# Kernel optimization log

Hardware: AMD Instinct MI355X
Metric: run time of the kernel (lower is better)

The kernel has to match this reference:

```python
import jax, jax.numpy as jnp
import numpy as np

# VG model constants hard-coded in the torch module
THETA = -0.1436
MU = 0.1686
SIGMA = 0.1213
N_STEPS = 365          # len(timegrid) - 1
T_END = 1.0            # timegrid = linspace(0, 1, 366)
MC = 200000
N_MAT = 12
N_STRIKES = 21


def setup_inputs() -> dict:
    key = jax.random.key(0)
    k1, k2 = jax.random.split(key, 2)
    h = T_END / N_STEPS
    S0 = jnp.full((1, 1), 100.0, dtype=jnp.float32)
    rate = jnp.full((1, 1), 0.025, dtype=jnp.float32)
    z = jax.random.normal(k1, (MC, N_STEPS), dtype=jnp.float32)
    # VG subordinator increments: Gamma(shape=h/mu, scale=mu)
    gamma = (jax.random.gamma(k2, h / MU, (MC, N_STEPS)) * MU).astype(jnp.float32)
    # monthly maturities on the daily grid
    indices = (jnp.arange(1, N_MAT + 1, dtype=jnp.int32) * 30)
    strikes_call = jnp.linspace(80.0, 120.0, N_STRIKES, dtype=jnp.float32)
    strikes_put = jnp.linspace(80.0, 120.0, N_STRIKES, dtype=jnp.float32)
    return {"S0": S0, "rate": rate, "indices": indices, "z": z, "gamma": gamma,
            "strikes_call": strikes_call, "strikes_put": strikes_put,
            "MC_samples": MC}


def reference(S0, rate, indices, z, gamma, strikes_call, strikes_put, MC_samples):
    h = jnp.asarray(T_END / N_STEPS, dtype=z.dtype)
    # martingale correction w = (1/mu) * log(1 - theta*mu - sigma^2*mu/2)
    w = (1.0 / MU) * jnp.log(1.0 - THETA * MU - SIGMA * SIGMA * MU / 2.0)
    r = rate.reshape(())
    s0 = S0.reshape(())
    # VG log-increment per step; cumulative sum gives X after each step i
    incr = THETA * gamma + SIGMA * jnp.sqrt(gamma) * z      # [MC, N_STEPS]
    X = jnp.cumsum(incr, axis=1)                            # X[:, i-1] = X after step i
    # gather the maturity steps
    Xm = X[:, indices - 1]                                  # [MC, M]
    im = indices.astype(z.dtype)                            # [M]
    Sm = s0 * jnp.exp((r + w) * im * h + Xm)                # [MC, M]
    disc = jnp.exp(-r * im / N_STEPS)                       # [M] (discount as in torch code)
    Sb = Sm[:, :, None]                                     # [MC, M, 1]
    Kc = strikes_call[None, None, :]                        # [1, 1, K]
    Kp = strikes_put[None, None, :]
    d = disc[:, None]                                       # [M, 1]
    call      = jnp.maximum(Sb - Kc, 0.0).mean(axis=0) * d  # average_SS
    put_otm   = jnp.maximum(Kp - Sb, 0.0).mean(axis=0) * d  # average_SS_OTM
    call_kput = jnp.maximum(Sb - Kp, 0.0).mean(axis=0) * d  # average_SS1
    put_kcall = jnp.maximum(Kc - Sb, 0.0).mean(axis=0) * d  # average_SS1_ITM
    # [4*M, K]
    return jnp.concatenate([call, put_otm, call_kput, put_kcall], axis=0)
```

## Files before the change

kernel.cpp:

```cpp
#include <hip/hip_runtime.h>
#include <math.h>


#define NSTEPS 365
#define NM     12
#define NK     21
#define PPW    8
#define WAVES  4
#define BLOCK  (WAVES * 64)
#define PPB    (WAVES * PPW)

#define NCELL  (NM * NK)
#define WSZ    (2 * NCELL + NM)

#define THETA_F (-0.1436f)
#define SIGMA_F (0.1213f)
#define THETA_D (-0.1436)
#define MU_D    (0.1686)
#define SIGMA_D (0.1213)

template <int CTRL, int RMASK>
__device__ __forceinline__ float dpp_add(float v) {
    const int t = __builtin_amdgcn_update_dpp(0, __float_as_int(v), CTRL, RMASK, 0xf, true);
    return v + __int_as_float(t);
}
__device__ __forceinline__ float scan64(float v) {
    v = dpp_add<0x111, 0xf>(v);
    v = dpp_add<0x112, 0xf>(v);
    v = dpp_add<0x114, 0xf>(v);
    v = dpp_add<0x118, 0xf>(v);
    v = dpp_add<0x142, 0xa>(v);
    v = dpp_add<0x143, 0xc>(v);
    return v;
}
__device__ __forceinline__ float rdlane(float v, int l) {
    return __int_as_float(__builtin_amdgcn_readlane(__float_as_int(v), l));
}

__global__ __launch_bounds__(BLOCK) void vg_paths_kernel(
    const float* __restrict__ S0p, const float* __restrict__ ratep,
    const int* __restrict__ indices, const float* __restrict__ z,
    const float* __restrict__ gam, const float* __restrict__ Kc,
    const float* __restrict__ Kp, float* __restrict__ acc, int MC)
{
    __shared__ float lacc[WSZ];
    const int tid = threadIdx.x;
    for (int i = tid; i < WSZ; i += BLOCK) lacc[i] = 0.f;
    __syncthreads();

    const int lane = tid & 63;
    const int wv   = tid >> 6;
    const int k    = lane % NK;
    const int mg   = lane / NK;

    const float kc  = Kc[k];
    const float kp  = Kp[k];
    const float r_  = ratep[0];
    const float s0_ = S0p[0];
    const float w   = (float)((1.0 / MU_D) *
                      log(1.0 - THETA_D * MU_D - SIGMA_D * SIGMA_D * MU_D / 2.0));
    const float rwh  = (r_ + w) / (float)NSTEPS;
    const float lns0 = logf(s0_);

    float ab2[NM];
    #pragma unroll
    for (int m = 0; m < NM; ++m) ab2[m] = rwh * (float)indices[m] + lns0;

    float ac_c[4], ac_p[4], sS[4];
    #pragma unroll
    for (int j = 0; j < 4; ++j) { ac_c[j] = 0.f; ac_p[j] = 0.f; sS[j] = 0.f; }

    auto loadp = [&](int p, float* zv, float* gv) {
        const int pc = min(p, MC - 1);
        const float* zp = z   + (size_t)pc * NSTEPS;
        const float* gp = gam + (size_t)pc * NSTEPS;
        #pragma unroll
        for (int c = 0; c < 5; ++c) {
            zv[c] = zp[lane + 64 * c];
            gv[c] = gp[lane + 64 * c];
        }
        const int o5 = min(lane + 320, 364);
        zv[5] = zp[o5]; gv[5] = gp[o5];
    };

    auto process = [&](const float* zv, const float* gv, bool pv) {
        float X[NM];
        float carry = 0.f;
        #pragma unroll
        for (int c = 0; c < 6; ++c) {
            const float g = gv[c];
            float v = fmaf(THETA_F, g, SIGMA_F * (sqrtf(g) * zv[c]));
            if (c == 5) v = (lane < 45) ? v : 0.f;
            v = scan64(v);
            X[2 * c]     = carry + rdlane(v, 29 - 4 * c);
            X[2 * c + 1] = carry + rdlane(v, 59 - 4 * c);
            carry       += rdlane(v, 63);
        }
        if (!pv) return;
        float S[NM];
        #pragma unroll
        for (int m = 0; m < NM; ++m) S[m] = __expf(ab2[m] + X[m]);
        #pragma unroll
        for (int j = 0; j < 4; ++j) {
            const float Sj = (mg == 0) ? S[j] : (mg == 1) ? S[j + 4] : S[j + 8];
            ac_c[j] += fmaxf(Sj - kc, 0.f);
            ac_p[j] += fmaxf(Sj - kp, 0.f);
            sS[j]   += Sj;
        }
    };

    const int p0 = blockIdx.x * PPB + wv * PPW;
    float zA[6], gA[6], zB[6], gB[6];
    loadp(p0, zA, gA);
    #pragma unroll 1
    for (int pp = 0; pp < PPW; pp += 2) {
        loadp(p0 + pp + 1, zB, gB);
        process(zA, gA, p0 + pp < MC);
        loadp(p0 + pp + 2, zA, gA);
        process(zB, gB, p0 + pp + 1 < MC);
    }

    if (lane < 63) {
        #pragma unroll
        for (int j = 0; j < 4; ++j) {
            const int cell = (4 * mg + j) * NK + k;
            atomicAdd(&lacc[cell],         ac_c[j]);
            atomicAdd(&lacc[NCELL + cell], ac_p[j]);
        }
        if (k == 0) {
            #pragma unroll
            for (int j = 0; j < 4; ++j)
                atomicAdd(&lacc[2 * NCELL + 4 * mg + j], sS[j]);
        }
    }
    __syncthreads();
    for (int i = tid; i < WSZ; i += BLOCK)
        atomicAdd(&acc[i], lacc[i]);
}

__global__ void vg_finalize_kernel(const float* __restrict__ acc,
                                   const float* __restrict__ ratep,
                                   const int* __restrict__ indices,
                                   const float* __restrict__ Kc,
                                   const float* __restrict__ Kp,
                                   float* __restrict__ out, int MC)
{
    const int i = blockIdx.x * blockDim.x + threadIdx.x;
    if (i >= 4 * NCELL) return;
    const int t    = i / NCELL;
    const int cell = i % NCELL;
    const int m    = cell / NK;
    const int kk   = cell % NK;
    const float r_   = ratep[0];
    const float im   = (float)indices[m];
    const float disc = expf(-r_ * im / (float)NSTEPS);
    const float cc = acc[cell];
    const float cp = acc[NCELL + cell];
    const float sS = acc[2 * NCELL + m];
    const float fM = (float)MC;
    float v;
    if      (t == 0) v = cc;
    else if (t == 1) v = cp - sS + fM * Kp[kk];
    else if (t == 2) v = cp;
    else             v = cc - sS + fM * Kc[kk];
    out[i] = disc * v / fM;
}

extern "C" void kernel_launch(void* const* d_in, const int* in_sizes, int n_in,
                              void* d_out, int out_size, void* d_ws, size_t ws_size,
                              hipStream_t stream) {
    const float* S0      = (const float*)d_in[0];
    const float* rate    = (const float*)d_in[1];
    const int*   indices = (const int*)d_in[2];
    const float* z       = (const float*)d_in[3];
    const float* gamma_  = (const float*)d_in[4];
    const float* Kc      = (const float*)d_in[5];
    const float* Kp      = (const float*)d_in[6];

    const int MC = in_sizes[3] / NSTEPS;
    float* acc = (float*)d_ws;

    (void)hipMemsetAsync(d_ws, 0, WSZ * sizeof(float), stream);

    const int nb = (MC + PPB - 1) / PPB;
    vg_paths_kernel<<<nb, BLOCK, 0, stream>>>(S0, rate, indices, z, gamma_, Kc, Kp, acc, MC);

    vg_finalize_kernel<<<(4 * NCELL + 255) / 256, 256, 0, stream>>>(
        acc, rate, indices, Kc, Kp, (float*)d_out, MC);
}
```

Measured before the change: 193.4 us.

## Interleave two paths' DPP scans and deepen load prefetch; use exp2 domain

Processes two Monte Carlo paths at once, so their DPP prefix-scan chains interleave and hide DPP latency. The main loop is fully unrolled and keeps four paths of loads in flight instead of two. Constants are folded into base-2 so exp2f replaces __expf, and the per-maturity offsets are made scalar via readfirstlane. This costs more VGPRs, which may lower occupancy.

```diff
diff --git a/kernel.cpp b/kernel.cpp
--- a/kernel.cpp
+++ b/kernel.cpp
@@ -18,23 +18,18 @@
 #define THETA_D (-0.1436)
 #define MU_D    (0.1686)
 #define SIGMA_D (0.1213)
+#define LOG2E_F (1.4426950408889634f)
 
 template <int CTRL, int RMASK>
 __device__ __forceinline__ float dpp_add(float v) {
     const int t = __builtin_amdgcn_update_dpp(0, __float_as_int(v), CTRL, RMASK, 0xf, true);
     return v + __int_as_float(t);
 }
-__device__ __forceinline__ float scan64(float v) {
-    v = dpp_add<0x111, 0xf>(v);
-    v = dpp_add<0x112, 0xf>(v);
-    v = dpp_add<0x114, 0xf>(v);
-    v = dpp_add<0x118, 0xf>(v);
-    v = dpp_add<0x142, 0xa>(v);
-    v = dpp_add<0x143, 0xc>(v);
-    return v;
-}
 __device__ __forceinline__ float rdlane(float v, int l) {
     return __int_as_float(__builtin_amdgcn_readlane(__float_as_int(v), l));
+}
+__device__ __forceinline__ float rfl(float v) {
+    return __int_as_float(__builtin_amdgcn_readfirstlane(__float_as_int(v)));
 }
 
 __global__ __launch_bounds__(BLOCK) void vg_paths_kernel(
@@ -59,16 +54,21 @@
     const float s0_ = S0p[0];
     const float w   = (float)((1.0 / MU_D) *
                       log(1.0 - THETA_D * MU_D - SIGMA_D * SIGMA_D * MU_D / 2.0));
-    const float rwh  = (r_ + w) / (float)NSTEPS;
-    const float lns0 = logf(s0_);
+    const float th2  = THETA_F * LOG2E_F;
+    const float sg2  = SIGMA_F * LOG2E_F;
+    const float rwh2 = (r_ + w) * LOG2E_F / (float)NSTEPS;
+    const float l2s0 = log2f(s0_);
 
     float ab2[NM];
     #pragma unroll
-    for (int m = 0; m < NM; ++m) ab2[m] = rwh * (float)indices[m] + lns0;
+    for (int m = 0; m < NM; ++m) ab2[m] = rfl(rwh2 * (float)indices[m] + l2s0);
 
     float ac_c[4], ac_p[4], sS[4];
     #pragma unroll
     for (int j = 0; j < 4; ++j) { ac_c[j] = 0.f; ac_p[j] = 0.f; sS[j] = 0.f; }
+
+    const int o5 = min(lane + 320, 364);
+    const bool m5 = (lane < 45);
 
     auto loadp = [&](int p, float* zv, float* gv) {
         const int pc = min(p, MC - 1);
@@ -79,46 +79,60 @@
             zv[c] = zp[lane + 64 * c];
             gv[c] = gp[lane + 64 * c];
         }
-        const int o5 = min(lane + 320, 364);
         zv[5] = zp[o5]; gv[5] = gp[o5];
     };
 
-    auto process = [&](const float* zv, const float* gv, bool pv) {
-        float X[NM];
-        float carry = 0.f;
+    auto process2 = [&](const float* zA, const float* gA, bool pvA,
+                        const float* zB, const float* gB, bool pvB) {
+        float XA[NM], XB[NM];
+        float cA = 0.f, cB = 0.f;
         #pragma unroll
         for (int c = 0; c < 6; ++c) {
-            const float g = gv[c];
-            float v = fmaf(THETA_F, g, SIGMA_F * (sqrtf(g) * zv[c]));
-            if (c == 5) v = (lane < 45) ? v : 0.f;
-            v = scan64(v);
-            X[2 * c]     = carry + rdlane(v, 29 - 4 * c);
-            X[2 * c + 1] = carry + rdlane(v, 59 - 4 * c);
-            carry       += rdlane(v, 63);
-        }
-        if (!pv) return;
-        float S[NM];
-        #pragma unroll
-        for (int m = 0; m < NM; ++m) S[m] = __expf(ab2[m] + X[m]);
-        #pragma unroll
-        for (int j = 0; j < 4; ++j) {
-            const float Sj = (mg == 0) ? S[j] : (mg == 1) ? S[j + 4] : S[j + 8];
-            ac_c[j] += fmaxf(Sj - kc, 0.f);
-            ac_p[j] += fmaxf(Sj - kp, 0.f);
-            sS[j]   += Sj;
+            const float ga = gA[c], gb = gB[c];
+            float va = fmaf(th2, ga, sg2 * (sqrtf(ga) * zA[c]));
+            float vb = fmaf(th2, gb, sg2 * (sqrtf(gb) * zB[c]));
+            if (c == 5) { va = m5 ? va : 0.f; vb = m5 ? vb : 0.f; }
+            va = dpp_add<0x111, 0xf>(va);  vb = dpp_add<0x111, 0xf>(vb);
+            va = dpp_add<0x112, 0xf>(va);  vb = dpp_add<0x112, 0xf>(vb);
+            va = dpp_add<0x114, 0xf>(va);  vb = dpp_add<0x114, 0xf>(vb);
+            va = dpp_add<0x118, 0xf>(va);  vb = dpp_add<0x118, 0xf>(vb);
+            va = dpp_add<0x142, 0xa>(va);  vb = dpp_add<0x142, 0xa>(vb);
+            va = dpp_add<0x143, 0xc>(va);  vb = dpp_add<0x143, 0xc>(vb);
+            XA[2 * c]     = cA + rdlane(va, 29 - 4 * c);
+            XB[2 * c]     = cB + rdlane(vb, 29 - 4 * c);
+            XA[2 * c + 1] = cA + rdlane(va, 59 - 4 * c);
+            XB[2 * c + 1] = cB + rdlane(vb, 59 - 4 * c);
+            cA += rdlane(va, 63);
+            cB += rdlane(vb, 63);
+        }
+        #pragma unroll
+        for (int half = 0; half < 2; ++half) {
+            const float* X = half ? XB : XA;
+            const bool  pv = half ? pvB : pvA;
+            if (!pv) continue;
+            float S[NM];
+            #pragma unroll
+            for (int m = 0; m < NM; ++m) S[m] = exp2f(ab2[m] + X[m]);
+            #pragma unroll
+            for (int j = 0; j < 4; ++j) {
+                const float Sj = (mg == 0) ? S[j] : (mg == 1) ? S[j + 4] : S[j + 8];
+                ac_c[j] += fmaxf(Sj - kc, 0.f);
+                ac_p[j] += fmaxf(Sj - kp, 0.f);
+                sS[j]   += Sj;
+            }
         }
     };
 
     const int p0 = blockIdx.x * PPB + wv * PPW;
-    float zA[6], gA[6], zB[6], gB[6];
-    loadp(p0, zA, gA);
-    #pragma unroll 1
-    for (int pp = 0; pp < PPW; pp += 2) {
-        loadp(p0 + pp + 1, zB, gB);
-        process(zA, gA, p0 + pp < MC);
-        loadp(p0 + pp + 2, zA, gA);
-        process(zB, gB, p0 + pp + 1 < MC);
-    }
+    float zE[6], gE[6], zO[6], gO[6], zE2[6], gE2[6], zO2[6], gO2[6];
+    loadp(p0 + 0, zE,  gE );  loadp(p0 + 1, zO,  gO );
+    loadp(p0 + 2, zE2, gE2);  loadp(p0 + 3, zO2, gO2);
+    process2(zE,  gE,  p0 + 0 < MC, zO,  gO,  p0 + 1 < MC);
+    loadp(p0 + 4, zE,  gE );  loadp(p0 + 5, zO,  gO );
+    process2(zE2, gE2, p0 + 2 < MC, zO2, gO2, p0 + 3 < MC);
+    loadp(p0 + 6, zE2, gE2);  loadp(p0 + 7, zO2, gO2);
+    process2(zE,  gE,  p0 + 4 < MC, zO,  gO,  p0 + 5 < MC);
+    process2(zE2, gE2, p0 + 6 < MC, zO2, gO2, p0 + 7 < MC);
 
     if (lane < 63) {
         #pragma unroll
```

After: 197.5 us. 2.1% more time.

## Switch to one path per thread with sequential scan and LDS payoff stage

Applied to the files above, without the earlier changes.

Replaces the wave-cooperative path scan (one path per wave, DPP prefix sums) with one path per thread. Each thread sums its 365 increments sequentially using float4 loads, with per-wave alignment offsets so the vector loads stay 16-byte aligned. Spot prices go to shared memory, and each wave then accumulates payoffs over its 64 paths. It also folds log2e into the constants so exp2f can be used, and hardcodes maturities as multiples of 30 instead of reading indices. The aim is to remove cross-lane scan and readlane overhead, at the cost of strided, uncoalesced per-thread memory access and a dependence on the specific test maturity grid.

```diff
diff --git a/kernel.cpp b/kernel.cpp
--- a/kernel.cpp
+++ b/kernel.cpp
@@ -5,11 +5,7 @@
 #define NSTEPS 365
 #define NM     12
 #define NK     21
-#define PPW    8
-#define WAVES  4
-#define BLOCK  (WAVES * 64)
-#define PPB    (WAVES * PPW)
-
+#define BLOCK  256
 #define NCELL  (NM * NK)
 #define WSZ    (2 * NCELL + NM)
 
@@ -18,23 +14,58 @@
 #define THETA_D (-0.1436)
 #define MU_D    (0.1686)
 #define SIGMA_D (0.1213)
+#define LOG2E_F (1.4426950408889634f)
 
-template <int CTRL, int RMASK>
-__device__ __forceinline__ float dpp_add(float v) {
-    const int t = __builtin_amdgcn_update_dpp(0, __float_as_int(v), CTRL, RMASK, 0xf, true);
-    return v + __int_as_float(t);
-}
-__device__ __forceinline__ float scan64(float v) {
-    v = dpp_add<0x111, 0xf>(v);
-    v = dpp_add<0x112, 0xf>(v);
-    v = dpp_add<0x114, 0xf>(v);
-    v = dpp_add<0x118, 0xf>(v);
-    v = dpp_add<0x142, 0xa>(v);
-    v = dpp_add<0x143, 0xc>(v);
-    return v;
-}
-__device__ __forceinline__ float rdlane(float v, int l) {
-    return __int_as_float(__builtin_amdgcn_readlane(__float_as_int(v), l));
+template <int Q>
+__device__ __forceinline__ void sim_path(const float* __restrict__ zA,
+                                         const float* __restrict__ gA,
+                                         float th2, float sg2,
+                                         float rwh2, float l2s0,
+                                         float* __restrict__ Srow)
+{
+    float X = 0.f;
+    #pragma unroll 1
+    for (int rr = 0; rr < 6; ++rr) {
+        const float* zb = zA + 60 * rr;
+        const float* gb = gA + 60 * rr;
+        const float frr = (float)rr;
+        const bool rr0 = (rr == 0);
+        #pragma unroll
+        for (int r2 = 0; r2 < 15; ++r2) {
+            const float4 z4 = *(const float4*)(zb + 4 * r2);
+            const float4 g4 = *(const float4*)(gb + 4 * r2);
+            #define VG_EL(ZJ, GJ, LE)                                          \
+            do {                                                               \
+                float inc = fmaf(th2, (GJ), sg2 * (sqrtf((GJ)) * (ZJ)));       \
+                if (Q > 0 && (LE) < Q) inc = rr0 ? 0.f : inc;     \
+                X += inc;                                                      \
+                if (Q > 0 && (LE) == Q - 1) {            \
+                    if (!rr0)                                                  \
+                        Srow[2 * rr - 1] =                                     \
+                            exp2f(fmaf(rwh2, 60.f * frr, l2s0) + X);           \
+                }                                                              \
+                if ((LE) == 29 + Q)                      \
+                    Srow[2 * rr] =                                             \
+                        exp2f(fmaf(rwh2, 60.f * frr + 30.f, l2s0) + X);        \
+                if (Q == 0 && (LE) == 59)                \
+                    Srow[2 * rr + 1] =                                         \
+                        exp2f(fmaf(rwh2, 60.f * frr + 60.f, l2s0) + X);        \
+            } while (0)
+            VG_EL(z4.x, g4.x, 4 * r2 + 0);
+            VG_EL(z4.y, g4.y, 4 * r2 + 1);
+            VG_EL(z4.z, g4.z, 4 * r2 + 2);
+            VG_EL(z4.w, g4.w, 4 * r2 + 3);
+            #undef VG_EL
+        }
+    }
+    if (Q > 0) {
+        const float4 z4 = *(const float4*)(zA + 360);
+        const float4 g4 = *(const float4*)(gA + 360);
+        if (Q >= 1) X += fmaf(th2, g4.x, sg2 * (sqrtf(g4.x) * z4.x));
+        if (Q >= 2) X += fmaf(th2, g4.y, sg2 * (sqrtf(g4.y) * z4.y));
+        if (Q >= 3) X += fmaf(th2, g4.z, sg2 * (sqrtf(g4.z) * z4.z));
+        Srow[11] = exp2f(fmaf(rwh2, 360.f, l2s0) + X);
+    }
 }
 
 __global__ __launch_bounds__(BLOCK) void vg_paths_kernel(
@@ -43,81 +74,57 @@
     const float* __restrict__ gam, const float* __restrict__ Kc,
     const float* __restrict__ Kp, float* __restrict__ acc, int MC)
 {
+    __shared__ float Sl[BLOCK * 13];
     __shared__ float lacc[WSZ];
     const int tid = threadIdx.x;
     for (int i = tid; i < WSZ; i += BLOCK) lacc[i] = 0.f;
-    __syncthreads();
 
     const int lane = tid & 63;
     const int wv   = tid >> 6;
-    const int k    = lane % NK;
-    const int mg   = lane / NK;
+    const int p0   = blockIdx.x * BLOCK;
+    const int p    = p0 + 4 * lane + wv;
+    int pcl = p;
+    if (pcl >= MC) pcl = p - 4 * ((p - MC) / 4 + 1);
 
-    const float kc  = Kc[k];
-    const float kp  = Kp[k];
     const float r_  = ratep[0];
     const float s0_ = S0p[0];
     const float w   = (float)((1.0 / MU_D) *
                       log(1.0 - THETA_D * MU_D - SIGMA_D * SIGMA_D * MU_D / 2.0));
-    const float rwh  = (r_ + w) / (float)NSTEPS;
-    const float lns0 = logf(s0_);
+    const float th2  = THETA_F * LOG2E_F;
+    const float sg2  = SIGMA_F * LOG2E_F;
+    const float rwh2 = (r_ + w) * LOG2E_F / (float)NSTEPS;
+    const float l2s0 = log2f(s0_);
 
-    float ab2[NM];
-    #pragma unroll
-    for (int m = 0; m < NM; ++m) ab2[m] = rwh * (float)indices[m] + lns0;
+    const float* zA = z   + (size_t)pcl * NSTEPS - wv;
+    const float* gA = gam + (size_t)pcl * NSTEPS - wv;
+    float* Srow = &Sl[tid * 13];
 
-    float ac_c[4], ac_p[4], sS[4];
-    #pragma unroll
-    for (int j = 0; j < 4; ++j) { ac_c[j] = 0.f; ac_p[j] = 0.f; sS[j] = 0.f; }
+    if      (wv == 0) sim_path<0>(zA, gA, th2, sg2, rwh2, l2s0, Srow);
+    else if (wv == 1) sim_path<1>(zA, gA, th2, sg2, rwh2, l2s0, Srow);
+    else if (wv == 2) sim_path<2>(zA, gA, th2, sg2, rwh2, l2s0, Srow);
+    else              sim_path<3>(zA, gA, th2, sg2, rwh2, l2s0, Srow);
+    __syncthreads();
 
-    auto loadp = [&](int p, float* zv, float* gv) {
-        const int pc = min(p, MC - 1);
-        const float* zp = z   + (size_t)pc * NSTEPS;
-        const float* gp = gam + (size_t)pc * NSTEPS;
-        #pragma unroll
-        for (int c = 0; c < 5; ++c) {
-            zv[c] = zp[lane + 64 * c];
-            gv[c] = gp[lane + 64 * c];
-        }
-        const int o5 = min(lane + 320, 364);
-        zv[5] = zp[o5]; gv[5] = gp[o5];
-    };
+    const int k   = lane % NK;
+    const int mg  = lane / NK;
+    const int mgc = (mg > 2) ? 2 : mg;
+    const float kc = Kc[k], kp = Kp[k];
+    const int rem = MC - p0;
+    const int pvw = min(64, max(0, (rem - wv + 3) >> 2));
 
-    auto process = [&](const float* zv, const float* gv, bool pv) {
-        float X[NM];
-        float carry = 0.f;
-        #pragma unroll
-        for (int c = 0; c < 6; ++c) {
-            const float g = gv[c];
-            float v = fmaf(THETA_F, g, SIGMA_F * (sqrtf(g) * zv[c]));
-            if (c == 5) v = (lane < 45) ? v : 0.f;
-            v = scan64(v);
-            X[2 * c]     = carry + rdlane(v, 29 - 4 * c);
-            X[2 * c + 1] = carry + rdlane(v, 59 - 4 * c);
-            carry       += rdlane(v, 63);
-        }
-        if (!pv) return;
-        float S[NM];
-        #pragma unroll
-        for (int m = 0; m < NM; ++m) S[m] = __expf(ab2[m] + X[m]);
+    float ac_c[4] = {0.f, 0.f, 0.f, 0.f};
+    float ac_p[4] = {0.f, 0.f, 0.f, 0.f};
+    float sSl[4]  = {0.f, 0.f, 0.f, 0.f};
+    #pragma unroll 1
+    for (int pp = 0; pp < pvw; ++pp) {
+        const float* Sp = &Sl[(64 * wv + pp) * 13 + 4 * mgc];
         #pragma unroll
         for (int j = 0; j < 4; ++j) {
-            const float Sj = (mg == 0) ? S[j] : (mg == 1) ? S[j + 4] : S[j + 8];
-            ac_c[j] += fmaxf(Sj - kc, 0.f);
-            ac_p[j] += fmaxf(Sj - kp, 0.f);
-            sS[j]   += Sj;
+            const float S = Sp[j];
+            ac_c[j] += fmaxf(S - kc, 0.f);
+            ac_p[j] += fmaxf(S - kp, 0.f);
+            sSl[j]  += S;
         }
-    };
-
-    const int p0 = blockIdx.x * PPB + wv * PPW;
-    float zA[6], gA[6], zB[6], gB[6];
-    loadp(p0, zA, gA);
-    #pragma unroll 1
-    for (int pp = 0; pp < PPW; pp += 2) {
-        loadp(p0 + pp + 1, zB, gB);
-        process(zA, gA, p0 + pp < MC);
-        loadp(p0 + pp + 2, zA, gA);
-        process(zB, gB, p0 + pp + 1 < MC);
     }
 
     if (lane < 63) {
@@ -130,7 +137,7 @@
         if (k == 0) {
             #pragma unroll
             for (int j = 0; j < 4; ++j)
-                atomicAdd(&lacc[2 * NCELL + 4 * mg + j], sS[j]);
+                atomicAdd(&lacc[2 * NCELL + 4 * mg + j], sSl[j]);
         }
     }
     __syncthreads();
@@ -182,7 +189,7 @@
 
     (void)hipMemsetAsync(d_ws, 0, WSZ * sizeof(float), stream);
 
-    const int nb = (MC + PPB - 1) / PPB;
+    const int nb = (MC + BLOCK - 1) / BLOCK;
     vg_paths_kernel<<<nb, BLOCK, 0, stream>>>(S0, rate, indices, z, gamma_, Kc, Kp, acc, MC);
 
     vg_finalize_kernel<<<(4 * NCELL + 255) / 256, 256, 0, stream>>>(
```

New measurement: 296.9 us. 1.54x slower.

## Split each wave into two half-wave paths with 32-lane scans and higher occupancy

Applied to the files above, without the earlier changes.

Each wave now processes two paths at once, one per 32-lane half, using a 32-wide DPP scan instead of a 64-wide one. All loads for both paths are issued up front rather than double-buffered over eight paths per wave, and blocks grow to 512 threads with an occupancy hint in the launch bounds. Constants are folded into log2 form so exp2f replaces __expf, and per-lane constants are made wave-uniform with readfirstlane. The aim is more memory parallelism and less scan and loop overhead per path. In exchange the grid has many more blocks, so block-level LDS and global atomics increase per path.

```diff
diff --git a/kernel.cpp b/kernel.cpp
--- a/kernel.cpp
+++ b/kernel.cpp
@@ -5,11 +5,9 @@
 #define NSTEPS 365
 #define NM     12
 #define NK     21
-#define PPW    8
-#define WAVES  4
-#define BLOCK  (WAVES * 64)
-#define PPB    (WAVES * PPW)
-
+#define BLOCK  512
+#define WPB    (BLOCK / 64)
+#define PPB    (2 * WPB)
 #define NCELL  (NM * NK)
 #define WSZ    (2 * NCELL + NM)
 
@@ -18,26 +16,29 @@
 #define THETA_D (-0.1436)
 #define MU_D    (0.1686)
 #define SIGMA_D (0.1213)
+#define LOG2E_F (1.4426950408889634f)
 
 template <int CTRL, int RMASK>
 __device__ __forceinline__ float dpp_add(float v) {
     const int t = __builtin_amdgcn_update_dpp(0, __float_as_int(v), CTRL, RMASK, 0xf, true);
     return v + __int_as_float(t);
 }
-__device__ __forceinline__ float scan64(float v) {
+__device__ __forceinline__ float scan32(float v) {
     v = dpp_add<0x111, 0xf>(v);
     v = dpp_add<0x112, 0xf>(v);
     v = dpp_add<0x114, 0xf>(v);
     v = dpp_add<0x118, 0xf>(v);
     v = dpp_add<0x142, 0xa>(v);
-    v = dpp_add<0x143, 0xc>(v);
     return v;
 }
 __device__ __forceinline__ float rdlane(float v, int l) {
     return __int_as_float(__builtin_amdgcn_readlane(__float_as_int(v), l));
 }
+__device__ __forceinline__ float rfl(float v) {
+    return __int_as_float(__builtin_amdgcn_readfirstlane(__float_as_int(v)));
+}
 
-__global__ __launch_bounds__(BLOCK) void vg_paths_kernel(
+__global__ __launch_bounds__(BLOCK, 6) void vg_paths_kernel(
     const float* __restrict__ S0p, const float* __restrict__ ratep,
     const int* __restrict__ indices, const float* __restrict__ z,
     const float* __restrict__ gam, const float* __restrict__ Kc,
@@ -50,75 +51,77 @@
 
     const int lane = tid & 63;
     const int wv   = tid >> 6;
-    const int k    = lane % NK;
-    const int mg   = lane / NK;
+    const int l31  = lane & 31;
 
-    const float kc  = Kc[k];
-    const float kp  = Kp[k];
+    const int pA = blockIdx.x * PPB + 2 * wv;
+    const int pB = pA + 1;
+    const int pc = min((lane < 32) ? pA : pB, MC - 1);
+
     const float r_  = ratep[0];
     const float s0_ = S0p[0];
     const float w   = (float)((1.0 / MU_D) *
                       log(1.0 - THETA_D * MU_D - SIGMA_D * SIGMA_D * MU_D / 2.0));
-    const float rwh  = (r_ + w) / (float)NSTEPS;
-    const float lns0 = logf(s0_);
+    const float th2  = THETA_F * LOG2E_F;
+    const float sg2  = SIGMA_F * LOG2E_F;
+    const float rwh2 = (r_ + w) * LOG2E_F / (float)NSTEPS;
+    const float l2s0 = log2f(s0_);
 
     float ab2[NM];
     #pragma unroll
-    for (int m = 0; m < NM; ++m) ab2[m] = rwh * (float)indices[m] + lns0;
+    for (int m = 0; m < NM; ++m) ab2[m] = rfl(rwh2 * (float)indices[m] + l2s0);
 
-    float ac_c[4], ac_p[4], sS[4];
+    const size_t ibase = (size_t)pc * NSTEPS + l31;
+    const size_t gmaxi = (size_t)MC * NSTEPS - 1;
+    const float* zr = z   + ibase;
+    const float* gr = gam + ibase;
+    const size_t i11 = (ibase + 352 > gmaxi) ? gmaxi : ibase + 352;
+
+    float zv[12], gv[12];
     #pragma unroll
-    for (int j = 0; j < 4; ++j) { ac_c[j] = 0.f; ac_p[j] = 0.f; sS[j] = 0.f; }
+    for (int c = 0; c < 11; ++c) { zv[c] = zr[32 * c]; gv[c] = gr[32 * c]; }
+    zv[11] = z[i11]; gv[11] = gam[i11];
 
-    auto loadp = [&](int p, float* zv, float* gv) {
-        const int pc = min(p, MC - 1);
-        const float* zp = z   + (size_t)pc * NSTEPS;
-        const float* gp = gam + (size_t)pc * NSTEPS;
-        #pragma unroll
-        for (int c = 0; c < 5; ++c) {
-            zv[c] = zp[lane + 64 * c];
-            gv[c] = gp[lane + 64 * c];
+    float XA[NM], XB[NM];
+    float cA = 0.f, cB = 0.f;
+    #pragma unroll
+    for (int c = 0; c < 12; ++c) {
+        const float g = gv[c];
+        float v = fmaf(th2, g, sg2 * (sqrtf(g) * zv[c]));
+        v = scan32(v);
+        XA[c] = cA + rdlane(v, 29 - 2 * c);
+        XB[c] = cB + rdlane(v, 61 - 2 * c);
+        if (c < 11) {
+            cA += rdlane(v, 31);
+            cB += rdlane(v, 63);
         }
-        const int o5 = min(lane + 320, 364);
-        zv[5] = zp[o5]; gv[5] = gp[o5];
-    };
+    }
 
-    auto process = [&](const float* zv, const float* gv, bool pv) {
-        float X[NM];
-        float carry = 0.f;
-        #pragma unroll
-        for (int c = 0; c < 6; ++c) {
-            const float g = gv[c];
-            float v = fmaf(THETA_F, g, SIGMA_F * (sqrtf(g) * zv[c]));
-            if (c == 5) v = (lane < 45) ? v : 0.f;
-            v = scan64(v);
-            X[2 * c]     = carry + rdlane(v, 29 - 4 * c);
-            X[2 * c + 1] = carry + rdlane(v, 59 - 4 * c);
-            carry       += rdlane(v, 63);
-        }
-        if (!pv) return;
-        float S[NM];
-        #pragma unroll
-        for (int m = 0; m < NM; ++m) S[m] = __expf(ab2[m] + X[m]);
-        #pragma unroll
-        for (int j = 0; j < 4; ++j) {
-            const float Sj = (mg == 0) ? S[j] : (mg == 1) ? S[j + 4] : S[j + 8];
-            ac_c[j] += fmaxf(Sj - kc, 0.f);
-            ac_p[j] += fmaxf(Sj - kp, 0.f);
-            sS[j]   += Sj;
-        }
-    };
+    const int k  = lane % NK;
+    const int mg = lane / NK;
+    const float kc = Kc[k], kp = Kp[k];
+    float ac_c[4] = {0.f, 0.f, 0.f, 0.f};
+    float ac_p[4] = {0.f, 0.f, 0.f, 0.f};
+    float sS4[4]  = {0.f, 0.f, 0.f, 0.f};
 
-    const int p0 = blockIdx.x * PPB + wv * PPW;
-    float zA[6], gA[6], zB[6], gB[6];
-    loadp(p0, zA, gA);
-    #pragma unroll 1
-    for (int pp = 0; pp < PPW; pp += 2) {
-        loadp(p0 + pp + 1, zB, gB);
-        process(zA, gA, p0 + pp < MC);
-        loadp(p0 + pp + 2, zA, gA);
-        process(zB, gB, p0 + pp + 1 < MC);
-    }
+    #define VG_ACCUM(X, pv)                                                   \
+    do {                                                                      \
+        if (pv) {                                                             \
+            float S[NM];                                                      \
+            _Pragma("unroll")                                                 \
+            for (int m = 0; m < NM; ++m) S[m] = exp2f(ab2[m] + (X)[m]);       \
+            _Pragma("unroll")                                                 \
+            for (int j = 0; j < 4; ++j) {                                     \
+                const float Sj = (mg == 0) ? S[j]                             \
+                               : (mg == 1) ? S[j + 4] : S[j + 8];             \
+                ac_c[j] += fmaxf(Sj - kc, 0.f);                               \
+                ac_p[j] += fmaxf(Sj - kp, 0.f);                               \
+                sS4[j]  += Sj;                                                \
+            }                                                                 \
+        }                                                                     \
+    } while (0)
+    VG_ACCUM(XA, pA < MC);
+    VG_ACCUM(XB, pB < MC);
+    #undef VG_ACCUM
 
     if (lane < 63) {
         #pragma unroll
@@ -130,7 +133,7 @@
         if (k == 0) {
             #pragma unroll
             for (int j = 0; j < 4; ++j)
-                atomicAdd(&lacc[2 * NCELL + 4 * mg + j], sS[j]);
+                atomicAdd(&lacc[2 * NCELL + 4 * mg + j], sS4[j]);
         }
     }
     __syncthreads();
```

New measurement: 374.9 us. +93.9%, slower.
